# Kernel optimization log

Measured on AMD Instinct MI355X. Metric: run time of the kernel, lower is better.

Reference implementation:

```python
import jax, jax.numpy as jnp
import numpy as np
from jax.scipy.special import logsumexp

B, T, D, L = 64, 512, 1024, 16


def setup_inputs() -> dict:
    key = jax.random.key(0)
    ks = jax.random.split(key, 6)
    x = jax.random.normal(ks[0], (B, T, D), dtype=jnp.float32)
    mask = jnp.ones((B, T), dtype=bool)
    labels = jax.random.randint(ks[1], (B, T), 0, L)
    W = jax.random.normal(ks[2], (D, L), dtype=jnp.float32) * (1.0 / np.sqrt(D))
    b = jnp.zeros((L,), dtype=jnp.float32)
    transitions = jax.random.normal(ks[3], (L, L), dtype=jnp.float32) * 0.1
    start_trans = jax.random.normal(ks[4], (L,), dtype=jnp.float32) * 0.1
    end_trans = jax.random.normal(ks[5], (L,), dtype=jnp.float32) * 0.1
    return {"x": x, "mask": mask, "labels": labels, "W": W, "b": b,
            "transitions": transitions, "start_trans": start_trans, "end_trans": end_trans}


def _crf_loss(x, mask, labels, W, b, transitions, start_trans, end_trans):
    logits = jnp.einsum("btd,dl->btl", x, W) + b  # (B,T,L)
    maskf = mask.astype(logits.dtype)

    # ---- log partition via forward algorithm (scan over time) ----
    logits_t = jnp.swapaxes(logits, 0, 1)  # (T,B,L)
    mask_t = jnp.swapaxes(mask, 0, 1)      # (T,B)
    alpha0 = start_trans + logits_t[0]     # (B,L)

    def step(alpha, inp):
        emit, m = inp  # emit: (B,L), m: (B,)
        # transitions[i,j]: from tag i to tag j
        inner = alpha[:, :, None] + transitions[None, :, :] + emit[:, None, :]
        new = logsumexp(inner, axis=1)
        alpha = jnp.where(m[:, None], new, alpha)
        return alpha, None

    alpha, _ = jax.lax.scan(step, alpha0, (logits_t[1:], mask_t[1:]))
    log_z = logsumexp(alpha + end_trans, axis=-1)  # (B,)

    # ---- joint score of gold path ----
    emit = jnp.take_along_axis(logits, labels[..., None], axis=2)[..., 0]  # (B,T)
    emit_score = jnp.sum(emit * maskf, axis=1)
    trans = transitions[labels[:, :-1], labels[:, 1:]]  # (B,T-1)
    trans_score = jnp.sum(trans * maskf[:, 1:], axis=1)
    last_idx = jnp.sum(mask.astype(jnp.int32), axis=1) - 1  # (B,)
    last_tag = jnp.take_along_axis(labels, last_idx[:, None], axis=1)[:, 0]
    score = start_trans[labels[:, 0]] + emit_score + trans_score + end_trans[last_tag]

    log_likelihood = jnp.sum(score - log_z)
    return -log_likelihood  # loss


def reference(x, mask, labels, W, b, transitions, start_trans, end_trans):
    return _crf_loss(x, mask, labels, W, b, transitions, start_trans, end_trans)
```

## Files before the change

### kernel.cpp

```cpp
#include <hip/hip_runtime.h>

#define B_ 64
#define T_ 512
#define D_ 1024
#define L_ 16
#define NPROD 2048

typedef __attribute__((ext_vector_type(8))) short short8;
typedef __attribute__((ext_vector_type(4))) float f32x4;
typedef __attribute__((ext_vector_type(4))) float fvec4;

__device__ __forceinline__ unsigned bfpack(float lo, float hi) {
    unsigned a = __float_as_uint(lo), b = __float_as_uint(hi);
    a = (a + 0x7FFFu + ((a >> 16) & 1u)) >> 16;
    b = (b + 0x7FFFu + ((b >> 16) & 1u)) & 0xFFFF0000u;
    return a | b;
}

__device__ __forceinline__ void store_f32_sc(float* p, float v) {
    asm volatile("global_store_dword %0, %1, off sc0 sc1" :: "v"(p), "v"(v) : "memory");
}
__device__ __forceinline__ unsigned load_u32_sc(const unsigned* p) {
    unsigned v;
    asm volatile("global_load_dword %0, %1, off sc0 sc1\n\ts_waitcnt vmcnt(0)"
                 : "=v"(v) : "v"(p) : "memory");
    return v;
}
__device__ __forceinline__ float load_f32_sc(const float* p) {
    float v;
    asm volatile("global_load_dword %0, %1, off sc0 sc1\n\ts_waitcnt vmcnt(0)"
                 : "=v"(v) : "v"(p) : "memory");
    return v;
}

__global__ __launch_bounds__(256, 2) void crf_fused(
        const float* __restrict__ x, const int* __restrict__ labels,
        const float* __restrict__ W, const float* __restrict__ bias,
        const float* __restrict__ trans, const float* __restrict__ startt,
        const float* __restrict__ endt, float* __restrict__ logits,
        unsigned* __restrict__ flags, unsigned* __restrict__ cnt,
        float* __restrict__ partials, float* __restrict__ out, int fused) {
    constexpr int LDU = 1040;
    constexpr int XS_BYTES = 16 * LDU * 2;
    __shared__ __align__(16) unsigned char raw[XS_BYTES + 4 * 16 * 16 * 4];
    const int tid = threadIdx.x;

    if (blockIdx.x < NPROD) {
        unsigned short* xs = (unsigned short*)raw;
        float (*part)[16][16] = (float (*)[16][16])(raw + XS_BYTES);
        const int l    = tid & 63;
        const int kq   = tid >> 6;
        const int quad = l >> 4;
        const int m    = l & 15;
        const int r0   = blockIdx.x * 16;
        if (!fused && blockIdx.x == 0 && tid == 0) out[0] = 0.f;

        const fvec4* gx = reinterpret_cast<const fvec4*>(x + (size_t)r0 * D_);
        fvec4 stg[16];
#pragma unroll
        for (int i = 0; i < 16; ++i) {
            asm volatile("global_load_dwordx4 %0, %1, off sc0 sc1 nt"
                         : "=&v"(stg[i])
                         : "v"(gx + i * 256 + tid)
                         : "memory");
        }

        uint4 wf[8];
#pragma unroll
        for (int c = 0; c < 8; ++c) {
            const int k0 = kq * 256 + c * 32 + quad * 8;
            unsigned u0 = bfpack(W[(size_t)(k0 + 0) * L_ + m], W[(size_t)(k0 + 1) * L_ + m]);
            unsigned u1 = bfpack(W[(size_t)(k0 + 2) * L_ + m], W[(size_t)(k0 + 3) * L_ + m]);
            unsigned u2 = bfpack(W[(size_t)(k0 + 4) * L_ + m], W[(size_t)(k0 + 5) * L_ + m]);
            unsigned u3 = bfpack(W[(size_t)(k0 + 6) * L_ + m], W[(size_t)(k0 + 7) * L_ + m]);
            wf[c] = make_uint4(u0, u1, u2, u3);
        }

        asm volatile("s_waitcnt vmcnt(0)" ::: "memory");
        __builtin_amdgcn_sched_barrier(0);

#pragma unroll
        for (int i = 0; i < 16; ++i) {
            unsigned u0 = bfpack(stg[i].x, stg[i].y);
            unsigned u1 = bfpack(stg[i].z, stg[i].w);
            *reinterpret_cast<uint2*>(&xs[i * LDU + 4 * tid]) = make_uint2(u0, u1);
        }
        __syncthreads();

        f32x4 acc = {0.f, 0.f, 0.f, 0.f};
#pragma unroll
        for (int c = 0; c < 8; ++c) {
            const unsigned short* xr = &xs[m * LDU + (kq * 8 + c) * 32 + quad * 8];
            union { uint2 v[2]; short8 s; } a;
            a.v[0] = *reinterpret_cast<const uint2*>(xr);
            a.v[1] = *reinterpret_cast<const uint2*>(xr + 4);
            union { uint4 u; short8 s; } bfr;
            bfr.u = wf[c];
            acc = __builtin_amdgcn_mfma_f32_16x16x32_bf16(a.s, bfr.s, acc, 0, 0, 0);
        }
#pragma unroll
        for (int r = 0; r < 4; ++r) part[kq][quad * 4 + r][m] = acc[r];
        __syncthreads();

        const int row = tid >> 4, col = tid & 15;
        float s = part[0][row][col] + part[1][row][col] + part[2][row][col] +
                  part[3][row][col] + bias[col];
        if (fused) {
            store_f32_sc(&logits[(size_t)(r0 + row) * L_ + col], s);
            asm volatile("s_waitcnt vmcnt(0)" ::: "memory");
            __syncthreads();
            if (tid == 0) {
                asm volatile("global_store_dword %0, %1, off sc0 sc1"
                             :: "v"(flags + blockIdx.x), "v"(1u) : "memory");
            }
        } else {
            logits[(size_t)(r0 + row) * L_ + col] = s;
        }
        return;
    }

    const int b = blockIdx.x - NPROD;
    float (*P)[256]  = (float (*)[256])raw;
    float* Ss        = (float*)(raw + 4096);
    float* scoreP    = (float*)(raw + 4096 + 16);
    const int w  = tid >> 6;
    const int l  = tid & 63;
    const int i  = l & 15;
    const int jq = l >> 4;
    const float* lg = logits + (size_t)b * (T_ * L_);

    float4 etp[4][4];
#pragma unroll
    for (int g = 0; g < 4; ++g)
#pragma unroll
        for (int t = 0; t < 4; ++t) {
            int k = ((jq ^ g) << 2) + t;
            float4 tv = *reinterpret_cast<const float4*>(&trans[k * L_ + (jq << 2)]);
            etp[g][t] = make_float4(__expf(tv.x), __expf(tv.y), __expf(tv.z), __expf(tv.w));
        }

    {
        const unsigned* f = flags + 32 * b + 8 * w;
        for (;;) {
            unsigned v = 1;
            if (l < 8) v = load_u32_sc(f + l);
            if (__all(v != 0)) break;
            __builtin_amdgcn_s_sleep(8);
        }
    }

    float p0 = (i == (jq << 2) + 0) ? 1.f : 0.f;
    float p1 = (i == (jq << 2) + 1) ? 1.f : 0.f;
    float p2 = (i == (jq << 2) + 2) ? 1.f : 0.f;
    float p3 = (i == (jq << 2) + 3) ? 1.f : 0.f;
    float S = 0.f;

    const int t0 = w * 128;
    float4 emn = *reinterpret_cast<const float4*>(&lg[(size_t)t0 * L_ + (jq << 2)]);
#pragma unroll 4
    for (int s = 0; s < 128; ++s) {
        float4 em = emn;
        if (s < 127)
            emn = *reinterpret_cast<const float4*>(&lg[(size_t)(t0 + s + 1) * L_ + (jq << 2)]);
        if (t0 + s >= 1) {
            float mx = fmaxf(fmaxf(em.x, em.y), fmaxf(em.z, em.w));
            mx = fmaxf(mx, __shfl_xor(mx, 16));
            mx = fmaxf(mx, __shfl_xor(mx, 32));
            S += mx;
            float qx = __expf(em.x - mx), qy = __expf(em.y - mx);
            float qz = __expf(em.z - mx), qw = __expf(em.w - mx);
            float r[4][4];
            r[0][0] = p0; r[0][1] = p1; r[0][2] = p2; r[0][3] = p3;
#pragma unroll
            for (int g = 1; g < 4; ++g) {
                r[g][0] = __shfl_xor(p0, g << 4);
                r[g][1] = __shfl_xor(p1, g << 4);
                r[g][2] = __shfl_xor(p2, g << 4);
                r[g][3] = __shfl_xor(p3, g << 4);
            }
            float ax = 0.f, ay = 0.f, az = 0.f, aw = 0.f;
#pragma unroll
            for (int g = 0; g < 4; ++g)
#pragma unroll
                for (int t = 0; t < 4; ++t) {
                    ax = fmaf(r[g][t], etp[g][t].x, ax);
                    ay = fmaf(r[g][t], etp[g][t].y, ay);
                    az = fmaf(r[g][t], etp[g][t].z, az);
                    aw = fmaf(r[g][t], etp[g][t].w, aw);
                }
            ax *= qx; ay *= qy; az *= qz; aw *= qw;
            if ((s & 3) == 3) {
                float m = fmaxf(fmaxf(ax, ay), fmaxf(az, aw));
#pragma unroll
                for (int ww = 1; ww < 64; ww <<= 1) m = fmaxf(m, __shfl_xor(m, ww));
                unsigned eb = (__float_as_uint(m) >> 23) & 0xFFu;
                float scl = __uint_as_float((254u - eb) << 23);
                ax *= scl; ay *= scl; az *= scl; aw *= scl;
                S += ((int)eb - 127) * 0.69314718056f;
            }
            p0 = ax; p1 = ay; p2 = az; p3 = aw;
        }
    }
    *reinterpret_cast<float4*>(&P[w][i * 16 + (jq << 2)]) = make_float4(p0, p1, p2, p3);
    if (l == 0) Ss[w] = S;

    {
        int t1 = t0 + l, t2 = t0 + 64 + l;
        int lt1 = labels[b * T_ + t1];
        float sc = lg[t1 * L_ + lt1];
        if (t1 >= 1) sc += trans[labels[b * T_ + t1 - 1] * L_ + lt1];
        int lt2 = labels[b * T_ + t2];
        sc += lg[t2 * L_ + lt2] + trans[labels[b * T_ + t2 - 1] * L_ + lt2];
#pragma unroll
        for (int ww = 1; ww < 64; ww <<= 1) sc += __shfl_xor(sc, ww);
        if (l == 0) scoreP[w] = sc;
    }
    __syncthreads();

    if (w == 0) {
        const int j = l & 15;
        const int kq = l >> 4;
        float a0 = startt[j] + lg[j];
        float m0 = a0;
#pragma unroll
        for (int ww = 1; ww < 16; ww <<= 1) m0 = fmaxf(m0, __shfl_xor(m0, ww));
        float v = __expf(a0 - m0);
        float S2 = m0;
        for (int c = 0; c < 4; ++c) {
            float cur[4];
#pragma unroll
            for (int t = 0; t < 4; ++t) cur[t] = P[c][(kq * 4 + t) * 16 + j];
            float pt = 0.f;
#pragma unroll
            for (int t = 0; t < 4; ++t)
                pt = fmaf(__shfl(v, (l & 48) + kq * 4 + t), cur[t], pt);
            pt += __shfl_xor(pt, 16);
            pt += __shfl_xor(pt, 32);
            S2 += Ss[c];
            if ((c & 3) == 3) {
                float m = pt;
#pragma unroll
                for (int ww = 1; ww < 16; ww <<= 1) m = fmaxf(m, __shfl_xor(m, ww));
                unsigned eb = (__float_as_uint(m) >> 23) & 0xFFu;
                pt *= __uint_as_float((254u - eb) << 23);
                S2 += ((int)eb - 127) * 0.69314718056f;
            }
            v = pt;
        }
        float term = v * __expf(endt[j]);
#pragma unroll
        for (int ww = 1; ww < 16; ww <<= 1) term += __shfl_xor(term, ww);
        float logz = S2 + __logf(term);

        int oldv = -1;
        if (l == 0) {
            float score = startt[labels[b * T_]] + endt[labels[b * T_ + T_ - 1]];
            score += scoreP[0] + scoreP[1] + scoreP[2] + scoreP[3];
            store_f32_sc(&partials[b], logz - score);
            asm volatile("s_waitcnt vmcnt(0)" ::: "memory");
            oldv = (int)atomicAdd(cnt, 1u);
        }
        oldv = __shfl(oldv, 0);
        if (oldv == B_ - 1) {
            float pv = load_f32_sc(&partials[l]);
#pragma unroll
            for (int ww = 1; ww < 64; ww <<= 1) pv += __shfl_xor(pv, ww);
            if (l == 0) out[0] = pv;
        }
    }
}

__global__ __launch_bounds__(1024) void crf_rest(const float* __restrict__ logits,
                                                 const int* __restrict__ labels,
                                                 const float* __restrict__ trans,
                                                 const float* __restrict__ startt,
                                                 const float* __restrict__ endt,
                                                 float* __restrict__ out) {
    __shared__ float P[16][256];
    __shared__ float Ss[16];
    __shared__ float scoreP[16];
    const int b = blockIdx.x;
    const int tid = threadIdx.x;
    const int w = tid >> 6;
    const int l = tid & 63;
    const int i = l & 15;
    const int jq = l >> 4;
    const float* lg = logits + (size_t)b * (T_ * L_);
    float4 etp[4][4];
#pragma unroll
    for (int g = 0; g < 4; ++g)
#pragma unroll
        for (int t = 0; t < 4; ++t) {
            int k = ((jq ^ g) << 2) + t;
            float4 tv = *reinterpret_cast<const float4*>(&trans[k * L_ + (jq << 2)]);
            etp[g][t] = make_float4(__expf(tv.x), __expf(tv.y), __expf(tv.z), __expf(tv.w));
        }
    float p0 = (i == (jq << 2) + 0) ? 1.f : 0.f;
    float p1 = (i == (jq << 2) + 1) ? 1.f : 0.f;
    float p2 = (i == (jq << 2) + 2) ? 1.f : 0.f;
    float p3 = (i == (jq << 2) + 3) ? 1.f : 0.f;
    float S = 0.f;
    const int t0 = w * 32;
    float4 emn = *reinterpret_cast<const float4*>(&lg[(size_t)t0 * L_ + (jq << 2)]);
#pragma unroll 4
    for (int s = 0; s < 32; ++s) {
        float4 em = emn;
        if (s < 31)
            emn = *reinterpret_cast<const float4*>(&lg[(size_t)(t0 + s + 1) * L_ + (jq << 2)]);
        if (t0 + s >= 1) {
            float mx = fmaxf(fmaxf(em.x, em.y), fmaxf(em.z, em.w));
            mx = fmaxf(mx, __shfl_xor(mx, 16));
            mx = fmaxf(mx, __shfl_xor(mx, 32));
            S += mx;
            float qx = __expf(em.x - mx), qy = __expf(em.y - mx);
            float qz = __expf(em.z - mx), qw = __expf(em.w - mx);
            float r[4][4];
            r[0][0] = p0; r[0][1] = p1; r[0][2] = p2; r[0][3] = p3;
#pragma unroll
            for (int g = 1; g < 4; ++g) {
                r[g][0] = __shfl_xor(p0, g << 4);
                r[g][1] = __shfl_xor(p1, g << 4);
                r[g][2] = __shfl_xor(p2, g << 4);
                r[g][3] = __shfl_xor(p3, g << 4);
            }
            float ax = 0.f, ay = 0.f, az = 0.f, aw = 0.f;
#pragma unroll
            for (int g = 0; g < 4; ++g)
#pragma unroll
                for (int t = 0; t < 4; ++t) {
                    ax = fmaf(r[g][t], etp[g][t].x, ax);
                    ay = fmaf(r[g][t], etp[g][t].y, ay);
                    az = fmaf(r[g][t], etp[g][t].z, az);
                    aw = fmaf(r[g][t], etp[g][t].w, aw);
                }
            ax *= qx; ay *= qy; az *= qz; aw *= qw;
            if ((s & 3) == 3) {
                float m = fmaxf(fmaxf(ax, ay), fmaxf(az, aw));
#pragma unroll
                for (int ww = 1; ww < 64; ww <<= 1) m = fmaxf(m, __shfl_xor(m, ww));
                unsigned eb = (__float_as_uint(m) >> 23) & 0xFFu;
                float scl = __uint_as_float((254u - eb) << 23);
                ax *= scl; ay *= scl; az *= scl; aw *= scl;
                S += ((int)eb - 127) * 0.69314718056f;
            }
            p0 = ax; p1 = ay; p2 = az; p3 = aw;
        }
    }
    *reinterpret_cast<float4*>(&P[w][i * 16 + (jq << 2)]) = make_float4(p0, p1, p2, p3);
    if (l == 0) Ss[w] = S;
    float sc = 0.f;
    if (tid < T_) {
        int lt = labels[b * T_ + tid];
        sc = lg[tid * L_ + lt];
        if (tid >= 1) sc += trans[labels[b * T_ + tid - 1] * L_ + lt];
    }
#pragma unroll
    for (int ww = 1; ww < 64; ww <<= 1) sc += __shfl_xor(sc, ww);
    if (l == 0) scoreP[w] = sc;
    __syncthreads();
    if (w == 0) {
        const int j = l & 15;
        const int kq = l >> 4;
        float a0 = startt[j] + lg[j];
        float m0 = a0;
#pragma unroll
        for (int ww = 1; ww < 16; ww <<= 1) m0 = fmaxf(m0, __shfl_xor(m0, ww));
        float v = __expf(a0 - m0);
        float S2 = m0;
        for (int c = 0; c < 16; ++c) {
            float cur[4];
#pragma unroll
            for (int t = 0; t < 4; ++t) cur[t] = P[c][(kq * 4 + t) * 16 + j];
            float pt = 0.f;
#pragma unroll
            for (int t = 0; t < 4; ++t)
                pt = fmaf(__shfl(v, (l & 48) + kq * 4 + t), cur[t], pt);
            pt += __shfl_xor(pt, 16);
            pt += __shfl_xor(pt, 32);
            S2 += Ss[c];
            if ((c & 3) == 3) {
                float m = pt;
#pragma unroll
                for (int ww = 1; ww < 16; ww <<= 1) m = fmaxf(m, __shfl_xor(m, ww));
                unsigned eb = (__float_as_uint(m) >> 23) & 0xFFu;
                pt *= __uint_as_float((254u - eb) << 23);
                S2 += ((int)eb - 127) * 0.69314718056f;
            }
            v = pt;
        }
        float term = v * __expf(endt[j]);
#pragma unroll
        for (int ww = 1; ww < 16; ww <<= 1) term += __shfl_xor(term, ww);
        float logz = S2 + __logf(term);
        if (l == 0) {
            float score = startt[labels[b * T_]] + endt[labels[b * T_ + T_ - 1]];
#pragma unroll
            for (int q = 0; q < 16; ++q) score += scoreP[q];
            atomicAdd(out, logz - score);
        }
    }
}

extern "C" void kernel_launch(void* const* d_in, const int* in_sizes, int n_in,
                              void* d_out, int out_size, void* d_ws, size_t ws_size,
                              hipStream_t stream) {
    const float* x      = (const float*)d_in[0];
    const int*   labels = (const int*)d_in[2];
    const float* W      = (const float*)d_in[3];
    const float* bias   = (const float*)d_in[4];
    const float* trans  = (const float*)d_in[5];
    const float* startt = (const float*)d_in[6];
    const float* endt   = (const float*)d_in[7];

    float*    logits   = (float*)d_ws;
    const size_t LOG_B = (size_t)B_ * T_ * L_ * 4;
    unsigned* flags    = (unsigned*)((char*)d_ws + LOG_B);
    unsigned* cnt      = flags + NPROD;
    float*    partials = (float*)(cnt + 1);
    float*    out      = (float*)d_out;
    const size_t need  = LOG_B + (NPROD + 1 + B_) * 4;

    if (ws_size >= need) {
        hipMemsetAsync(flags, 0, (NPROD + 1) * 4, stream);
        crf_fused<<<NPROD + B_, 256, 0, stream>>>(x, labels, W, bias, trans,
                                                  startt, endt, logits, flags,
                                                  cnt, partials, out, 1);
    } else {
        crf_fused<<<NPROD, 256, 0, stream>>>(x, labels, W, bias, trans,
                                             startt, endt, logits, flags,
                                             cnt, partials, out, 0);
        crf_rest<<<B_, 1024, 0, stream>>>(logits, labels, trans, startt, endt, out);
    }
}
```

Measured before the change: 246.2 us.

## Cut register pressure: split x staging, load W per-iteration, move exp(trans) to LDS

Producer blocks now stage x in two halves of 8 vector loads instead of 16, and convert W to bf16 inside a non-unrolled MFMA loop instead of keeping all 8 fragments in registers. Consumer blocks keep the exponentiated transition table in shared memory, read on every scan step, instead of 64 registers. The launch bound drops the min-2-blocks hint. The aim is lower VGPR use and higher occupancy, paid for with serialized load phases, repeated W global loads in the loop, and LDS reads on the latency-critical recurrence.

Result: slower. 318.3 us (+29.3%).

```diff
diff --git a/kernel.cpp b/kernel.cpp
--- a/kernel.cpp
+++ b/kernel.cpp
@@ -33,7 +33,7 @@
     return v;
 }
 
-__global__ __launch_bounds__(256, 2) void crf_fused(
+__global__ __launch_bounds__(256) void crf_fused(
         const float* __restrict__ x, const int* __restrict__ labels,
         const float* __restrict__ W, const float* __restrict__ bias,
         const float* __restrict__ trans, const float* __restrict__ startt,
@@ -44,11 +44,11 @@
     constexpr int XS_BYTES = 16 * LDU * 2;
     __shared__ __align__(16) unsigned char raw[XS_BYTES + 4 * 16 * 16 * 4];
     const int tid = threadIdx.x;
+    const int l   = tid & 63;
 
     if (blockIdx.x < NPROD) {
         unsigned short* xs = (unsigned short*)raw;
         float (*part)[16][16] = (float (*)[16][16])(raw + XS_BYTES);
-        const int l    = tid & 63;
         const int kq   = tid >> 6;
         const int quad = l >> 4;
         const int m    = l & 15;
@@ -56,47 +56,48 @@
         if (!fused && blockIdx.x == 0 && tid == 0) out[0] = 0.f;
 
         const fvec4* gx = reinterpret_cast<const fvec4*>(x + (size_t)r0 * D_);
-        fvec4 stg[16];
-#pragma unroll
-        for (int i = 0; i < 16; ++i) {
+        fvec4 stg[8];
+#pragma unroll
+        for (int i = 0; i < 8; ++i)
             asm volatile("global_load_dwordx4 %0, %1, off sc0 sc1 nt"
-                         : "=&v"(stg[i])
-                         : "v"(gx + i * 256 + tid)
-                         : "memory");
-        }
-
-        uint4 wf[8];
-#pragma unroll
+                         : "=&v"(stg[i]) : "v"(gx + i * 256 + tid) : "memory");
+        asm volatile("s_waitcnt vmcnt(0)" ::: "memory");
+        __builtin_amdgcn_sched_barrier(0);
+#pragma unroll
+        for (int i = 0; i < 8; ++i) {
+            unsigned u0 = bfpack(stg[i].x, stg[i].y);
+            unsigned u1 = bfpack(stg[i].z, stg[i].w);
+            *reinterpret_cast<uint2*>(&xs[i * LDU + 4 * tid]) = make_uint2(u0, u1);
+        }
+#pragma unroll
+        for (int i = 0; i < 8; ++i)
+            asm volatile("global_load_dwordx4 %0, %1, off sc0 sc1 nt"
+                         : "=&v"(stg[i]) : "v"(gx + (i + 8) * 256 + tid) : "memory");
+        asm volatile("s_waitcnt vmcnt(0)" ::: "memory");
+        __builtin_amdgcn_sched_barrier(0);
+#pragma unroll
+        for (int i = 0; i < 8; ++i) {
+            unsigned u0 = bfpack(stg[i].x, stg[i].y);
+            unsigned u1 = bfpack(stg[i].z, stg[i].w);
+            *reinterpret_cast<uint2*>(&xs[(i + 8) * LDU + 4 * tid]) = make_uint2(u0, u1);
+        }
+        __syncthreads();
+
+        f32x4 acc = {0.f, 0.f, 0.f, 0.f};
+#pragma unroll 1
         for (int c = 0; c < 8; ++c) {
+            const unsigned short* xr = &xs[m * LDU + (kq * 8 + c) * 32 + quad * 8];
+            union { uint2 v[2]; short8 s; } a;
+            a.v[0] = *reinterpret_cast<const uint2*>(xr);
+            a.v[1] = *reinterpret_cast<const uint2*>(xr + 4);
             const int k0 = kq * 256 + c * 32 + quad * 8;
             unsigned u0 = bfpack(W[(size_t)(k0 + 0) * L_ + m], W[(size_t)(k0 + 1) * L_ + m]);
             unsigned u1 = bfpack(W[(size_t)(k0 + 2) * L_ + m], W[(size_t)(k0 + 3) * L_ + m]);
             unsigned u2 = bfpack(W[(size_t)(k0 + 4) * L_ + m], W[(size_t)(k0 + 5) * L_ + m]);
             unsigned u3 = bfpack(W[(size_t)(k0 + 6) * L_ + m], W[(size_t)(k0 + 7) * L_ + m]);
-            wf[c] = make_uint4(u0, u1, u2, u3);
-        }
-
-        asm volatile("s_waitcnt vmcnt(0)" ::: "memory");
-        __builtin_amdgcn_sched_barrier(0);
-
-#pragma unroll
-        for (int i = 0; i < 16; ++i) {
-            unsigned u0 = bfpack(stg[i].x, stg[i].y);
-            unsigned u1 = bfpack(stg[i].z, stg[i].w);
-            *reinterpret_cast<uint2*>(&xs[i * LDU + 4 * tid]) = make_uint2(u0, u1);
-        }
-        __syncthreads();
-
-        f32x4 acc = {0.f, 0.f, 0.f, 0.f};
-#pragma unroll
-        for (int c = 0; c < 8; ++c) {
-            const unsigned short* xr = &xs[m * LDU + (kq * 8 + c) * 32 + quad * 8];
-            union { uint2 v[2]; short8 s; } a;
-            a.v[0] = *reinterpret_cast<const uint2*>(xr);
-            a.v[1] = *reinterpret_cast<const uint2*>(xr + 4);
-            union { uint4 u; short8 s; } bfr;
-            bfr.u = wf[c];
-            acc = __builtin_amdgcn_mfma_f32_16x16x32_bf16(a.s, bfr.s, acc, 0, 0, 0);
+            union { uint4 u; short8 s; } b;
+            b.u = make_uint4(u0, u1, u2, u3);
+            acc = __builtin_amdgcn_mfma_f32_16x16x32_bf16(a.s, b.s, acc, 0, 0, 0);
         }
 #pragma unroll
         for (int r = 0; r < 4; ++r) part[kq][quad * 4 + r][m] = acc[r];
@@ -122,22 +123,23 @@
     const int b = blockIdx.x - NPROD;
     float (*P)[256]  = (float (*)[256])raw;
     float* Ss        = (float*)(raw + 4096);
-    float* scoreP    = (float*)(raw + 4096 + 16);
+    float* scoreP    = (float*)(raw + 4096 + 64);
+    float4* etpB     = (float4*)(raw + 4224);
     const int w  = tid >> 6;
-    const int l  = tid & 63;
     const int i  = l & 15;
     const int jq = l >> 4;
     const float* lg = logits + (size_t)b * (T_ * L_);
-
-    float4 etp[4][4];
-#pragma unroll
-    for (int g = 0; g < 4; ++g)
-#pragma unroll
-        for (int t = 0; t < 4; ++t) {
-            int k = ((jq ^ g) << 2) + t;
-            float4 tv = *reinterpret_cast<const float4*>(&trans[k * L_ + (jq << 2)]);
-            etp[g][t] = make_float4(__expf(tv.x), __expf(tv.y), __expf(tv.z), __expf(tv.w));
-        }
+    float4* ew = etpB + w * 68;
+
+    {
+        int fj = l & 3, fg = (l >> 2) & 3, ft = l >> 4;
+        int k = ((fj ^ fg) << 2) + ft;
+        float4 tv = *reinterpret_cast<const float4*>(&trans[k * L_ + fj * 4]);
+        ew[fj * 17 + fg * 4 + ft] =
+            make_float4(__expf(tv.x), __expf(tv.y), __expf(tv.z), __expf(tv.w));
+    }
+    asm volatile("s_waitcnt lgkmcnt(0)" ::: "memory");
+    __builtin_amdgcn_sched_barrier(0);
 
     {
         const unsigned* f = flags + 32 * b + 8 * w;
@@ -178,15 +180,18 @@
                 r[g][2] = __shfl_xor(p2, g << 4);
                 r[g][3] = __shfl_xor(p3, g << 4);
             }
+            const float4* ewv = ew + jq * 17;
+            asm volatile("" : "+v"(ewv));
             float ax = 0.f, ay = 0.f, az = 0.f, aw = 0.f;
 #pragma unroll
             for (int g = 0; g < 4; ++g)
 #pragma unroll
                 for (int t = 0; t < 4; ++t) {
-                    ax = fmaf(r[g][t], etp[g][t].x, ax);
-                    ay = fmaf(r[g][t], etp[g][t].y, ay);
-                    az = fmaf(r[g][t], etp[g][t].z, az);
-                    aw = fmaf(r[g][t], etp[g][t].w, aw);
+                    float4 e = ewv[g * 4 + t];
+                    ax = fmaf(r[g][t], e.x, ax);
+                    ay = fmaf(r[g][t], e.y, ay);
+                    az = fmaf(r[g][t], e.z, az);
+                    aw = fmaf(r[g][t], e.w, aw);
                 }
             ax *= qx; ay *= qy; az *= qz; aw *= qw;
             if ((s & 3) == 3) {
```
